# Performance work log

Hardware: AMD Instinct MI355X
Metric: run time of the kernel (lower is better)

Reference implementation:

```python
import jax, jax.numpy as jnp
import numpy as np

N, E = 100000, 1600000
IN, HID, NCLS = 128, 128, 64


def setup_inputs() -> dict:
    key = jax.random.key(0)
    ks = jax.random.split(key, 8)
    x = jax.random.normal(ks[0], (N, IN), jnp.float32)
    edge_index = jax.random.randint(ks[1], (2, E), 0, N, dtype=jnp.int32)
    s1 = 1.0 / np.sqrt(IN)
    s2 = 1.0 / np.sqrt(HID)
    return {
        "x": x,
        "edge_index": edge_index,
        "Wl1": jax.random.uniform(ks[2], (IN, HID), jnp.float32, -s1, s1),
        "Wr1": jax.random.uniform(ks[3], (IN, HID), jnp.float32, -s1, s1),
        "b1": jnp.zeros((HID,), jnp.float32),
        "Wl2": jax.random.uniform(ks[4], (HID, NCLS), jnp.float32, -s2, s2),
        "Wr2": jax.random.uniform(ks[5], (HID, NCLS), jnp.float32, -s2, s2),
        "b2": jnp.zeros((NCLS,), jnp.float32),
    }


def _sage_conv(x, src, dst, inv_deg, Wl, Wr, b):
    # mean-aggregate neighbor features at each destination node (PyG SAGEConv)
    agg = jax.ops.segment_sum(x[src], dst, num_segments=N)  # [N, d]
    agg = agg * inv_deg[:, None]
    # out = lin_l(mean_j x_j) + lin_r(x_i); bias lives in lin_l
    return agg @ Wl + x @ Wr + b


def reference(x, edge_index, Wl1, Wr1, b1, Wl2, Wr2, b2):
    src, dst = edge_index[0], edge_index[1]
    deg = jax.ops.segment_sum(jnp.ones((E,), jnp.float32), dst, num_segments=N)
    inv_deg = 1.0 / jnp.maximum(deg, 1.0)
    h = _sage_conv(x, src, dst, inv_deg, Wl1, Wr1, b1)
    h = jax.nn.relu(h)
    # dropout is identity at inference (training=False)
    h = _sage_conv(h, src, dst, inv_deg, Wl2, Wr2, b2)
    return jax.nn.log_softmax(h, axis=1)
```

## Files before the change

### kernel.cpp

```cpp
#include <hip/hip_runtime.h>
#include <hip/hip_bf16.h>


typedef __attribute__((ext_vector_type(8))) short short8;
typedef __attribute__((ext_vector_type(4))) float f32x4;
typedef __attribute__((ext_vector_type(2))) float f32x2;

#define NPB 512
#define BCAP 16384
#define CHUNK 8192

__device__ __forceinline__ ushort f2bf(float f) {
    unsigned u = __float_as_uint(f);
    return (ushort)((u + 0x7fff + ((u >> 16) & 1)) >> 16);
}
__device__ __forceinline__ float bflo(unsigned v) { return __uint_as_float(v << 16); }
__device__ __forceinline__ float bfhi(unsigned v) { return __uint_as_float(v & 0xffff0000u); }
__device__ __forceinline__ unsigned pk4bf(float a, float b) {
    return (unsigned)f2bf(a) | ((unsigned)f2bf(b) << 16);
}

__global__ void bucket_scatter(const int* __restrict__ src, const int* __restrict__ dst,
                               int* __restrict__ bcount, unsigned* __restrict__ bbuf,
                               int E, int NB) {
    __shared__ unsigned entry[CHUNK];
    __shared__ unsigned char ebkt[CHUNK];
    __shared__ int lhist[256], lbase[256], lcur[256];
    int tid = threadIdx.x;
    lhist[tid] = 0;
    __syncthreads();
    int e0 = blockIdx.x * CHUNK;
    int cnt = min(CHUNK, E - e0);
    int nv = cnt >> 2;
    for (int t = tid; t < nv; t += 256) {
        int4 d4 = ((const int4*)(dst + e0))[t];
        int4 s4 = ((const int4*)(src + e0))[t];
        int i = t * 4;
        int b0 = d4.x >> 9, b1 = d4.y >> 9, b2 = d4.z >> 9, b3 = d4.w >> 9;
        entry[i + 0] = ((unsigned)s4.x << 9) | (unsigned)(d4.x & 511);
        entry[i + 1] = ((unsigned)s4.y << 9) | (unsigned)(d4.y & 511);
        entry[i + 2] = ((unsigned)s4.z << 9) | (unsigned)(d4.z & 511);
        entry[i + 3] = ((unsigned)s4.w << 9) | (unsigned)(d4.w & 511);
        ebkt[i + 0] = (unsigned char)b0; ebkt[i + 1] = (unsigned char)b1;
        ebkt[i + 2] = (unsigned char)b2; ebkt[i + 3] = (unsigned char)b3;
        atomicAdd(&lhist[b0], 1); atomicAdd(&lhist[b1], 1);
        atomicAdd(&lhist[b2], 1); atomicAdd(&lhist[b3], 1);
    }
    for (int i = (nv << 2) + tid; i < cnt; i += 256) {
        int d = dst[e0 + i], s = src[e0 + i];
        int b = d >> 9;
        entry[i] = ((unsigned)s << 9) | (unsigned)(d & 511);
        ebkt[i] = (unsigned char)b;
        atomicAdd(&lhist[b], 1);
    }
    __syncthreads();
    int h = lhist[tid];
    lbase[tid] = (h > 0) ? atomicAdd(&bcount[tid], h) : 0;
    lcur[tid] = 0;
    __syncthreads();
    for (int i = tid; i < cnt; i += 256) {
        int b = ebkt[i];
        int o = atomicAdd(&lcur[b], 1);
        bbuf[(long)b * BCAP + lbase[b] + o] = entry[i];
    }
}

__global__ void scan_buckets(const int* __restrict__ bcount, int* __restrict__ bbase, int NB) {
    __shared__ int s[256];
    int tid = threadIdx.x;
    int v = (tid < NB) ? bcount[tid] : 0;
    s[tid] = v;
    __syncthreads();
    for (int off = 1; off < 256; off <<= 1) {
        int a = (tid >= off) ? s[tid - off] : 0;
        __syncthreads();
        s[tid] += a;
        __syncthreads();
    }
    if (tid < NB) bbase[tid] = s[tid] - v;
}

__global__ void build_csr(const unsigned* __restrict__ bbuf, const int* __restrict__ bcount,
                          const int* __restrict__ bbase, int* __restrict__ row_start,
                          int* __restrict__ degw, float* __restrict__ inv_deg,
                          int* __restrict__ ssrc, int N) {
    __shared__ int sdeg[NPB], lcur[NPB];
    int b = blockIdx.x, tid = threadIdx.x;
    int node0 = b * NPB;
    sdeg[tid] = 0; sdeg[tid + 256] = 0;
    __syncthreads();
    int cnt = bcount[b];
    long base = (long)b * BCAP;
    for (int i = tid; i < cnt; i += 256)
        atomicAdd(&sdeg[bbuf[base + i] & 511], 1);
    __syncthreads();
    int c0 = sdeg[tid], c1 = sdeg[tid + 256];
    for (int off = 1; off < NPB; off <<= 1) {
        int a0 = (tid >= off) ? sdeg[tid - off] : 0;
        int a1 = (tid + 256 >= off) ? sdeg[tid + 256 - off] : 0;
        __syncthreads();
        sdeg[tid] += a0; sdeg[tid + 256] += a1;
        __syncthreads();
    }
    int bb = bbase[b];
    int rs0 = bb + sdeg[tid] - c0;
    int rs1 = bb + sdeg[tid + 256] - c1;
    lcur[tid] = rs0; lcur[tid + 256] = rs1;
    if (node0 + tid < N) {
        row_start[node0 + tid] = rs0;
        degw[node0 + tid] = c0;
        inv_deg[node0 + tid] = 1.0f / (float)(c0 > 1 ? c0 : 1);
    }
    if (node0 + tid + 256 < N) {
        row_start[node0 + tid + 256] = rs1;
        degw[node0 + tid + 256] = c1;
        inv_deg[node0 + tid + 256] = 1.0f / (float)(c1 > 1 ? c1 : 1);
    }
    __syncthreads();
    for (int i = tid; i < cnt; i += 256) {
        unsigned w = bbuf[base + i];
        int pos = atomicAdd(&lcur[w & 511], 1);
        ssrc[pos] = (int)(w >> 9);
    }
}

__device__ __forceinline__ void wfrag_one(const float* W, ushort* Wf, int i, int COLS) {
    int j = i & 7, m = (i >> 3) & 15, kc = (i >> 7) & 15, ct = i >> 11;
    Wf[i] = f2bf(W[(kc * 8 + j) * COLS + ct * 16 + m]);
}
__global__ void cvt_w_kernel(const float* __restrict__ Wl1, const float* __restrict__ Wr1,
                             const float* __restrict__ Wl2, const float* __restrict__ Wr2,
                             ushort* __restrict__ Wf_l1, ushort* __restrict__ Wf_r1,
                             ushort* __restrict__ Wf_l2, ushort* __restrict__ Wf_r2) {
    int i = blockIdx.x * blockDim.x + threadIdx.x;
    if (i < 16384)       wfrag_one(Wl1, Wf_l1, i, 128);
    else if (i < 32768)  wfrag_one(Wr1, Wf_r1, i - 16384, 128);
    else if (i < 40960)  wfrag_one(Wl2, Wf_l2, i - 32768, 64);
    else if (i < 49152)  wfrag_one(Wr2, Wf_r2, i - 40960, 64);
}

template <int COLS, bool F32IN>
__global__ void proj_kernel(const void* __restrict__ xin,
                            const ushort* __restrict__ Wfl, const ushort* __restrict__ Wfr,
                            const float* __restrict__ bias,
                            unsigned char* __restrict__ p8,
                            ushort* __restrict__ q,
                            int N) {
    constexpr int CT = COLS / 16;
    int wave = threadIdx.x >> 6, lane = threadIdx.x & 63;
    int quad = lane >> 4, m = lane & 15;
    long row0 = (long)blockIdx.x * 64 + wave * 16;
    long node = row0 + m;
    long arow = (node < N) ? node : (N - 1);

    f32x4 accp[CT], accq[CT];
#pragma unroll
    for (int ct = 0; ct < CT; ++ct) { accp[ct] = (f32x4)0.0f; accq[ct] = (f32x4)0.0f; }

#pragma unroll
    for (int kk = 0; kk < 128; kk += 32) {
        short8 b;
        if (F32IN) {
            const float* xf = (const float*)xin + arow * 128 + kk + quad * 8;
            float4 f0 = *(const float4*)xf;
            float4 f1 = *(const float4*)(xf + 4);
            b[0] = (short)f2bf(f0.x); b[1] = (short)f2bf(f0.y);
            b[2] = (short)f2bf(f0.z); b[3] = (short)f2bf(f0.w);
            b[4] = (short)f2bf(f1.x); b[5] = (short)f2bf(f1.y);
            b[6] = (short)f2bf(f1.z); b[7] = (short)f2bf(f1.w);
        } else {
            b = *(const short8*)((const ushort*)xin + arow * 128 + kk + quad * 8);
        }
        int kc = (kk >> 3) + quad;
#pragma unroll
        for (int ct = 0; ct < CT; ++ct) {
            long boff = (((long)(ct * 16 + kc) * 16) + m) * 8;
            short8 al = *(const short8*)(Wfl + boff);
            short8 ar = *(const short8*)(Wfr + boff);
            accp[ct] = __builtin_amdgcn_mfma_f32_16x16x32_bf16(al, b, accp[ct], 0, 0, 0);
            accq[ct] = __builtin_amdgcn_mfma_f32_16x16x32_bf16(ar, b, accq[ct], 0, 0, 0);
        }
    }

    if (node < N) {
#pragma unroll
        for (int ct = 0; ct < CT; ++ct) {
            int c0 = ct * 16 + quad * 4;
            float4 bv = *(const float4*)(bias + c0);
            float q0 = accq[ct][0] + bv.x, q1 = accq[ct][1] + bv.y;
            float q2 = accq[ct][2] + bv.z, q3 = accq[ct][3] + bv.w;
            unsigned w = (unsigned)__builtin_amdgcn_cvt_pk_fp8_f32(accp[ct][0], accp[ct][1], 0, false);
            w = (unsigned)__builtin_amdgcn_cvt_pk_fp8_f32(accp[ct][2], accp[ct][3], (int)w, true);
            *(unsigned*)(p8 + node * COLS + c0) = w;
            uint2 qw; qw.x = pk4bf(q0, q1); qw.y = pk4bf(q2, q3);
            *(uint2*)(q + node * COLS + c0) = qw;
        }
    }
}

__global__ void agg_relu_kernel(const unsigned char* __restrict__ p8,
                                const ushort* __restrict__ q,
                                const int* __restrict__ ssrc,
                                const int* __restrict__ row_start,
                                const int* __restrict__ deg,
                                const float* __restrict__ inv_deg,
                                ushort* __restrict__ hb, int N) {
    int wave = threadIdx.x >> 6, lane = threadIdx.x & 63;
    int n = blockIdx.x * 4 + wave;
    if (n >= N) return;
    int g = lane >> 4, lm = lane & 15;
    int start = row_start[n], d = deg[n];
    const int* sp = ssrc + start;
    const unsigned char* pb = p8 + lm * 8;
    float a[8] = {};
    int j = 0;
    for (; j + 16 <= d; j += 16) {
        int s0 = sp[j + g], s1 = sp[j + 4 + g], s2 = sp[j + 8 + g], s3 = sp[j + 12 + g];
        uint2 v0 = *(const uint2*)(pb + (long)s0 * 128);
        uint2 v1 = *(const uint2*)(pb + (long)s1 * 128);
        uint2 v2 = *(const uint2*)(pb + (long)s2 * 128);
        uint2 v3 = *(const uint2*)(pb + (long)s3 * 128);
#pragma unroll
        for (int t = 0; t < 4; ++t) {
            uint2 vv = (t == 0) ? v0 : (t == 1) ? v1 : (t == 2) ? v2 : v3;
            f32x2 c0 = __builtin_amdgcn_cvt_pk_f32_fp8((int)vv.x, false);
            f32x2 c1 = __builtin_amdgcn_cvt_pk_f32_fp8((int)vv.x, true);
            f32x2 c2 = __builtin_amdgcn_cvt_pk_f32_fp8((int)vv.y, false);
            f32x2 c3 = __builtin_amdgcn_cvt_pk_f32_fp8((int)vv.y, true);
            a[0] += c0[0]; a[1] += c0[1]; a[2] += c1[0]; a[3] += c1[1];
            a[4] += c2[0]; a[5] += c2[1]; a[6] += c3[0]; a[7] += c3[1];
        }
    }
    for (; j < d; j += 4) {
        int idx = j + g;
        int s = sp[idx < d ? idx : j];
        uint2 vv = *(const uint2*)(pb + (long)s * 128);
        if (idx < d) {
            f32x2 c0 = __builtin_amdgcn_cvt_pk_f32_fp8((int)vv.x, false);
            f32x2 c1 = __builtin_amdgcn_cvt_pk_f32_fp8((int)vv.x, true);
            f32x2 c2 = __builtin_amdgcn_cvt_pk_f32_fp8((int)vv.y, false);
            f32x2 c3 = __builtin_amdgcn_cvt_pk_f32_fp8((int)vv.y, true);
            a[0] += c0[0]; a[1] += c0[1]; a[2] += c1[0]; a[3] += c1[1];
            a[4] += c2[0]; a[5] += c2[1]; a[6] += c3[0]; a[7] += c3[1];
        }
    }
#pragma unroll
    for (int t = 0; t < 8; ++t) {
        a[t] += __shfl_xor(a[t], 16);
        a[t] += __shfl_xor(a[t], 32);
    }
    if (g == 0) {
        float iv = inv_deg[n];
        uint4 qv = *(const uint4*)(q + (long)n * 128 + lm * 8);
        float h0 = fmaxf(a[0] * iv + bflo(qv.x), 0.f);
        float h1 = fmaxf(a[1] * iv + bfhi(qv.x), 0.f);
        float h2 = fmaxf(a[2] * iv + bflo(qv.y), 0.f);
        float h3 = fmaxf(a[3] * iv + bfhi(qv.y), 0.f);
        float h4 = fmaxf(a[4] * iv + bflo(qv.z), 0.f);
        float h5 = fmaxf(a[5] * iv + bfhi(qv.z), 0.f);
        float h6 = fmaxf(a[6] * iv + bflo(qv.w), 0.f);
        float h7 = fmaxf(a[7] * iv + bfhi(qv.w), 0.f);
        uint4 hw;
        hw.x = pk4bf(h0, h1); hw.y = pk4bf(h2, h3);
        hw.z = pk4bf(h4, h5); hw.w = pk4bf(h6, h7);
        *(uint4*)(hb + (long)n * 128 + lm * 8) = hw;
    }
}

__global__ void agg_lsm_kernel(const unsigned char* __restrict__ u8,
                               const ushort* __restrict__ v,
                               const int* __restrict__ ssrc,
                               const int* __restrict__ row_start,
                               const int* __restrict__ deg,
                               const float* __restrict__ inv_deg,
                               float* __restrict__ out, int N) {
    int wave = threadIdx.x >> 6, lane = threadIdx.x & 63;
    int n = blockIdx.x * 4 + wave;
    if (n >= N) return;
    int g = lane >> 3, lm = lane & 7;
    int start = row_start[n], d = deg[n];
    const int* sp = ssrc + start;
    const unsigned char* ub = u8 + lm * 8;
    float a[8] = {};
    int j = 0;
    for (; j + 16 <= d; j += 16) {
        int s0 = sp[j + g], s1 = sp[j + 8 + g];
        uint2 v0 = *(const uint2*)(ub + (long)s0 * 64);
        uint2 v1 = *(const uint2*)(ub + (long)s1 * 64);
#pragma unroll
        for (int t = 0; t < 2; ++t) {
            uint2 vv = (t == 0) ? v0 : v1;
            f32x2 c0 = __builtin_amdgcn_cvt_pk_f32_fp8((int)vv.x, false);
            f32x2 c1 = __builtin_amdgcn_cvt_pk_f32_fp8((int)vv.x, true);
            f32x2 c2 = __builtin_amdgcn_cvt_pk_f32_fp8((int)vv.y, false);
            f32x2 c3 = __builtin_amdgcn_cvt_pk_f32_fp8((int)vv.y, true);
            a[0] += c0[0]; a[1] += c0[1]; a[2] += c1[0]; a[3] += c1[1];
            a[4] += c2[0]; a[5] += c2[1]; a[6] += c3[0]; a[7] += c3[1];
        }
    }
    for (; j < d; j += 8) {
        int idx = j + g;
        int s = sp[idx < d ? idx : j];
        uint2 vv = *(const uint2*)(ub + (long)s * 64);
        if (idx < d) {
            f32x2 c0 = __builtin_amdgcn_cvt_pk_f32_fp8((int)vv.x, false);
            f32x2 c1 = __builtin_amdgcn_cvt_pk_f32_fp8((int)vv.x, true);
            f32x2 c2 = __builtin_amdgcn_cvt_pk_f32_fp8((int)vv.y, false);
            f32x2 c3 = __builtin_amdgcn_cvt_pk_f32_fp8((int)vv.y, true);
            a[0] += c0[0]; a[1] += c0[1]; a[2] += c1[0]; a[3] += c1[1];
            a[4] += c2[0]; a[5] += c2[1]; a[6] += c3[0]; a[7] += c3[1];
        }
    }
#pragma unroll
    for (int t = 0; t < 8; ++t) {
        a[t] += __shfl_xor(a[t], 8);
        a[t] += __shfl_xor(a[t], 16);
        a[t] += __shfl_xor(a[t], 32);
    }
    float iv = inv_deg[n];
    uint4 vv = *(const uint4*)(v + (long)n * 64 + lm * 8);
    float z0 = a[0] * iv + bflo(vv.x), z1 = a[1] * iv + bfhi(vv.x);
    float z2 = a[2] * iv + bflo(vv.y), z3 = a[3] * iv + bfhi(vv.y);
    float z4 = a[4] * iv + bflo(vv.z), z5 = a[5] * iv + bfhi(vv.z);
    float z6 = a[6] * iv + bflo(vv.w), z7 = a[7] * iv + bfhi(vv.w);
    float mx = fmaxf(fmaxf(fmaxf(z0, z1), fmaxf(z2, z3)),
                     fmaxf(fmaxf(z4, z5), fmaxf(z6, z7)));
#pragma unroll
    for (int o = 4; o > 0; o >>= 1) mx = fmaxf(mx, __shfl_xor(mx, o));
    float e = (__expf(z0 - mx) + __expf(z1 - mx)) + (__expf(z2 - mx) + __expf(z3 - mx)) +
              (__expf(z4 - mx) + __expf(z5 - mx)) + (__expf(z6 - mx) + __expf(z7 - mx));
#pragma unroll
    for (int o = 4; o > 0; o >>= 1) e += __shfl_xor(e, o);
    float ls = mx + __logf(e);
    if (g == 0) {
        float4 o0, o1;
        o0.x = z0 - ls; o0.y = z1 - ls; o0.z = z2 - ls; o0.w = z3 - ls;
        o1.x = z4 - ls; o1.y = z5 - ls; o1.z = z6 - ls; o1.w = z7 - ls;
        *(float4*)(out + (long)n * 64 + lm * 8) = o0;
        *(float4*)(out + (long)n * 64 + lm * 8 + 4) = o1;
    }
}

extern "C" void kernel_launch(void* const* d_in, const int* in_sizes, int n_in,
                              void* d_out, int out_size, void* d_ws, size_t ws_size,
                              hipStream_t stream) {
    const float* x   = (const float*)d_in[0];
    const int*   ei  = (const int*)d_in[1];
    const float* Wl1 = (const float*)d_in[2];
    const float* Wr1 = (const float*)d_in[3];
    const float* b1  = (const float*)d_in[4];
    const float* Wl2 = (const float*)d_in[5];
    const float* Wr2 = (const float*)d_in[6];
    const float* b2  = (const float*)d_in[7];

    const int N = in_sizes[0] / 128;
    const int E = in_sizes[1] / 2;
    const int* src = ei;
    const int* dst = ei + E;
    const int NB = (N + NPB - 1) / NPB;

    size_t off = 0;
    auto take = [&](size_t nbytes) -> void* {
        void* ptr = (void*)((char*)d_ws + off);
        off += (nbytes + 255) & ~(size_t)255;
        return ptr;
    };
    int*      bcount    = (int*)take((size_t)NB * 4);
    int*      bbase     = (int*)take((size_t)NB * 4);
    unsigned* bbuf      = (unsigned*)take((size_t)NB * BCAP * 4);
    int*      row_start = (int*)take((size_t)N * 4);
    int*      degw      = (int*)take((size_t)N * 4);
    float*    inv_deg   = (float*)take((size_t)N * 4);
    int*      ssrc      = (int*)take((size_t)E * 4);
    unsigned char* p8   = (unsigned char*)take((size_t)N * 128);
    ushort*   q         = (ushort*)take((size_t)N * 128 * 2);
    ushort*   hb        = (ushort*)take((size_t)N * 128 * 2);
    ushort*   Wf_l1     = (ushort*)take(128 * 128 * 2);
    ushort*   Wf_r1     = (ushort*)take(128 * 128 * 2);
    ushort*   Wf_l2     = (ushort*)take(64 * 128 * 2);
    ushort*   Wf_r2     = (ushort*)take(64 * 128 * 2);
    unsigned char* u8 = p8;
    ushort*        v  = q;
    (void)ws_size; (void)n_in; (void)out_size;

    hipMemsetAsync(bcount, 0, (size_t)NB * 4, stream);

    bucket_scatter<<<(E + CHUNK - 1) / CHUNK, 256, 0, stream>>>(src, dst, bcount, bbuf, E, NB);
    scan_buckets  <<<1, 256, 0, stream>>>(bcount, bbase, NB);
    build_csr     <<<NB, 256, 0, stream>>>(bbuf, bcount, bbase, row_start, degw, inv_deg, ssrc, N);
    cvt_w_kernel  <<<192, 256, 0, stream>>>(Wl1, Wr1, Wl2, Wr2, Wf_l1, Wf_r1, Wf_l2, Wf_r2);

    proj_kernel<128, true><<<(N + 63) / 64, 256, 0, stream>>>(x, Wf_l1, Wf_r1, b1, p8, q, N);
    agg_relu_kernel<<<(N + 3) / 4, 256, 0, stream>>>(p8, q, ssrc, row_start, degw, inv_deg, hb, N);

    proj_kernel<64, false><<<(N + 63) / 64, 256, 0, stream>>>(hb, Wf_l2, Wf_r2, b2, u8, v, N);
    agg_lsm_kernel<<<(N + 3) / 4, 256, 0, stream>>>(u8, v, ssrc, row_start, degw, inv_deg,
                                                    (float*)d_out, N);
}
```

Baseline: 297.5 us.

## Widen gather loads to 16 bytes, shuffle-broadcast edge indices, merge scan with weight conversion

Both aggregation kernels now give each lane 16 fp8 features per 16-byte load, so fewer lanes cover a row and more edges are gathered per wave step. Each wave loads up to 64 neighbor indices in one coalesced read and hands them out with __shfl, replacing repeated scalar index loads. Accumulators become packed float2, and the bucket scan and weight-fragment conversion share one launch. The cost is more lanes idle on the masked tail for low-degree nodes, more shuffle reduction steps, and heavier per-lane epilogues.

```diff
diff --git a/kernel.cpp b/kernel.cpp
--- a/kernel.cpp
+++ b/kernel.cpp
@@ -18,6 +18,19 @@
 __device__ __forceinline__ float bfhi(unsigned v) { return __uint_as_float(v & 0xffff0000u); }
 __device__ __forceinline__ unsigned pk4bf(float a, float b) {
     return (unsigned)f2bf(a) | ((unsigned)f2bf(b) << 16);
+}
+__device__ __forceinline__ f32x2 shflx2(f32x2 v, int m) {
+    f32x2 r; r[0] = __shfl_xor(v[0], m); r[1] = __shfl_xor(v[1], m); return r;
+}
+__device__ __forceinline__ void acc16(uint4 v, f32x2* a) {
+    a[0] += __builtin_amdgcn_cvt_pk_f32_fp8((int)v.x, false);
+    a[1] += __builtin_amdgcn_cvt_pk_f32_fp8((int)v.x, true);
+    a[2] += __builtin_amdgcn_cvt_pk_f32_fp8((int)v.y, false);
+    a[3] += __builtin_amdgcn_cvt_pk_f32_fp8((int)v.y, true);
+    a[4] += __builtin_amdgcn_cvt_pk_f32_fp8((int)v.z, false);
+    a[5] += __builtin_amdgcn_cvt_pk_f32_fp8((int)v.z, true);
+    a[6] += __builtin_amdgcn_cvt_pk_f32_fp8((int)v.w, false);
+    a[7] += __builtin_amdgcn_cvt_pk_f32_fp8((int)v.w, true);
 }
 
 __global__ void bucket_scatter(const int* __restrict__ src, const int* __restrict__ dst,
@@ -65,19 +78,36 @@
     }
 }
 
-__global__ void scan_buckets(const int* __restrict__ bcount, int* __restrict__ bbase, int NB) {
-    __shared__ int s[256];
+__device__ __forceinline__ void wfrag_one(const float* W, ushort* Wf, int i, int COLS) {
+    int j = i & 7, m = (i >> 3) & 15, kc = (i >> 7) & 15, ct = i >> 11;
+    Wf[i] = f2bf(W[(kc * 8 + j) * COLS + ct * 16 + m]);
+}
+__global__ void scan_cvtw_kernel(const int* __restrict__ bcount, int* __restrict__ bbase,
+                                 int NB,
+                                 const float* __restrict__ Wl1, const float* __restrict__ Wr1,
+                                 const float* __restrict__ Wl2, const float* __restrict__ Wr2,
+                                 ushort* __restrict__ Wf_l1, ushort* __restrict__ Wf_r1,
+                                 ushort* __restrict__ Wf_l2, ushort* __restrict__ Wf_r2) {
     int tid = threadIdx.x;
-    int v = (tid < NB) ? bcount[tid] : 0;
-    s[tid] = v;
-    __syncthreads();
-    for (int off = 1; off < 256; off <<= 1) {
-        int a = (tid >= off) ? s[tid - off] : 0;
+    if (blockIdx.x == 0) {
+        __shared__ int s[256];
+        int v = (tid < NB) ? bcount[tid] : 0;
+        s[tid] = v;
         __syncthreads();
-        s[tid] += a;
-        __syncthreads();
-    }
-    if (tid < NB) bbase[tid] = s[tid] - v;
+        for (int off = 1; off < 256; off <<= 1) {
+            int a = (tid >= off) ? s[tid - off] : 0;
+            __syncthreads();
+            s[tid] += a;
+            __syncthreads();
+        }
+        if (tid < NB) bbase[tid] = s[tid] - v;
+        return;
+    }
+    int i = (int)(blockIdx.x - 1) * 256 + tid;
+    if (i < 16384)       wfrag_one(Wl1, Wf_l1, i, 128);
+    else if (i < 32768)  wfrag_one(Wr1, Wf_r1, i - 16384, 128);
+    else if (i < 40960)  wfrag_one(Wl2, Wf_l2, i - 32768, 64);
+    else if (i < 49152)  wfrag_one(Wr2, Wf_r2, i - 40960, 64);
 }
 
 __global__ void build_csr(const unsigned* __restrict__ bbuf, const int* __restrict__ bcount,
@@ -124,32 +154,16 @@
     }
 }
 
-__device__ __forceinline__ void wfrag_one(const float* W, ushort* Wf, int i, int COLS) {
-    int j = i & 7, m = (i >> 3) & 15, kc = (i >> 7) & 15, ct = i >> 11;
-    Wf[i] = f2bf(W[(kc * 8 + j) * COLS + ct * 16 + m]);
-}
-__global__ void cvt_w_kernel(const float* __restrict__ Wl1, const float* __restrict__ Wr1,
-                             const float* __restrict__ Wl2, const float* __restrict__ Wr2,
-                             ushort* __restrict__ Wf_l1, ushort* __restrict__ Wf_r1,
-                             ushort* __restrict__ Wf_l2, ushort* __restrict__ Wf_r2) {
-    int i = blockIdx.x * blockDim.x + threadIdx.x;
-    if (i < 16384)       wfrag_one(Wl1, Wf_l1, i, 128);
-    else if (i < 32768)  wfrag_one(Wr1, Wf_r1, i - 16384, 128);
-    else if (i < 40960)  wfrag_one(Wl2, Wf_l2, i - 32768, 64);
-    else if (i < 49152)  wfrag_one(Wr2, Wf_r2, i - 40960, 64);
-}
-
 template <int COLS, bool F32IN>
-__global__ void proj_kernel(const void* __restrict__ xin,
+__device__ __forceinline__ void proj_body(int bid, int tid,
+                            const void* __restrict__ xin,
                             const ushort* __restrict__ Wfl, const ushort* __restrict__ Wfr,
                             const float* __restrict__ bias,
-                            unsigned char* __restrict__ p8,
-                            ushort* __restrict__ q,
-                            int N) {
+                            unsigned char* __restrict__ p8, ushort* __restrict__ q, int N) {
     constexpr int CT = COLS / 16;
-    int wave = threadIdx.x >> 6, lane = threadIdx.x & 63;
+    int wave = tid >> 6, lane = tid & 63;
     int quad = lane >> 4, m = lane & 15;
-    long row0 = (long)blockIdx.x * 64 + wave * 16;
+    long row0 = (long)bid * 64 + wave * 16;
     long node = row0 + m;
     long arow = (node < N) ? node : (N - 1);
 
@@ -198,146 +212,153 @@
     }
 }
 
-__global__ void agg_relu_kernel(const unsigned char* __restrict__ p8,
-                                const ushort* __restrict__ q,
-                                const int* __restrict__ ssrc,
-                                const int* __restrict__ row_start,
-                                const int* __restrict__ deg,
-                                const float* __restrict__ inv_deg,
-                                ushort* __restrict__ hb, int N) {
-    int wave = threadIdx.x >> 6, lane = threadIdx.x & 63;
-    int n = blockIdx.x * 4 + wave;
-    if (n >= N) return;
-    int g = lane >> 4, lm = lane & 15;
-    int start = row_start[n], d = deg[n];
-    const int* sp = ssrc + start;
-    const unsigned char* pb = p8 + lm * 8;
-    float a[8] = {};
-    int j = 0;
-    for (; j + 16 <= d; j += 16) {
-        int s0 = sp[j + g], s1 = sp[j + 4 + g], s2 = sp[j + 8 + g], s3 = sp[j + 12 + g];
-        uint2 v0 = *(const uint2*)(pb + (long)s0 * 128);
-        uint2 v1 = *(const uint2*)(pb + (long)s1 * 128);
-        uint2 v2 = *(const uint2*)(pb + (long)s2 * 128);
-        uint2 v3 = *(const uint2*)(pb + (long)s3 * 128);
-#pragma unroll
-        for (int t = 0; t < 4; ++t) {
-            uint2 vv = (t == 0) ? v0 : (t == 1) ? v1 : (t == 2) ? v2 : v3;
-            f32x2 c0 = __builtin_amdgcn_cvt_pk_f32_fp8((int)vv.x, false);
-            f32x2 c1 = __builtin_amdgcn_cvt_pk_f32_fp8((int)vv.x, true);
-            f32x2 c2 = __builtin_amdgcn_cvt_pk_f32_fp8((int)vv.y, false);
-            f32x2 c3 = __builtin_amdgcn_cvt_pk_f32_fp8((int)vv.y, true);
-            a[0] += c0[0]; a[1] += c0[1]; a[2] += c1[0]; a[3] += c1[1];
-            a[4] += c2[0]; a[5] += c2[1]; a[6] += c3[0]; a[7] += c3[1];
-        }
-    }
-    for (; j < d; j += 4) {
-        int idx = j + g;
-        int s = sp[idx < d ? idx : j];
-        uint2 vv = *(const uint2*)(pb + (long)s * 128);
-        if (idx < d) {
-            f32x2 c0 = __builtin_amdgcn_cvt_pk_f32_fp8((int)vv.x, false);
-            f32x2 c1 = __builtin_amdgcn_cvt_pk_f32_fp8((int)vv.x, true);
-            f32x2 c2 = __builtin_amdgcn_cvt_pk_f32_fp8((int)vv.y, false);
-            f32x2 c3 = __builtin_amdgcn_cvt_pk_f32_fp8((int)vv.y, true);
-            a[0] += c0[0]; a[1] += c0[1]; a[2] += c1[0]; a[3] += c1[1];
-            a[4] += c2[0]; a[5] += c2[1]; a[6] += c3[0]; a[7] += c3[1];
-        }
-    }
-#pragma unroll
-    for (int t = 0; t < 8; ++t) {
-        a[t] += __shfl_xor(a[t], 16);
-        a[t] += __shfl_xor(a[t], 32);
-    }
-    if (g == 0) {
-        float iv = inv_deg[n];
-        uint4 qv = *(const uint4*)(q + (long)n * 128 + lm * 8);
-        float h0 = fmaxf(a[0] * iv + bflo(qv.x), 0.f);
-        float h1 = fmaxf(a[1] * iv + bfhi(qv.x), 0.f);
-        float h2 = fmaxf(a[2] * iv + bflo(qv.y), 0.f);
-        float h3 = fmaxf(a[3] * iv + bfhi(qv.y), 0.f);
-        float h4 = fmaxf(a[4] * iv + bflo(qv.z), 0.f);
-        float h5 = fmaxf(a[5] * iv + bfhi(qv.z), 0.f);
-        float h6 = fmaxf(a[6] * iv + bflo(qv.w), 0.f);
-        float h7 = fmaxf(a[7] * iv + bfhi(qv.w), 0.f);
-        uint4 hw;
-        hw.x = pk4bf(h0, h1); hw.y = pk4bf(h2, h3);
-        hw.z = pk4bf(h4, h5); hw.w = pk4bf(h6, h7);
-        *(uint4*)(hb + (long)n * 128 + lm * 8) = hw;
-    }
-}
-
-__global__ void agg_lsm_kernel(const unsigned char* __restrict__ u8,
-                               const ushort* __restrict__ v,
-                               const int* __restrict__ ssrc,
-                               const int* __restrict__ row_start,
-                               const int* __restrict__ deg,
-                               const float* __restrict__ inv_deg,
-                               float* __restrict__ out, int N) {
+__global__ void __launch_bounds__(256)
+proj1_kernel(const float* __restrict__ x,
+             const ushort* __restrict__ Wfl, const ushort* __restrict__ Wfr,
+             const float* __restrict__ bias,
+             unsigned char* __restrict__ p8, ushort* __restrict__ q, int N) {
+    proj_body<128, true>((int)blockIdx.x, (int)threadIdx.x, x, Wfl, Wfr, bias, p8, q, N);
+}
+__global__ void __launch_bounds__(256)
+proj2_kernel(const ushort* __restrict__ hb,
+             const ushort* __restrict__ Wfl, const ushort* __restrict__ Wfr,
+             const float* __restrict__ bias,
+             unsigned char* __restrict__ u8, ushort* __restrict__ v, int N) {
+    proj_body<64, false>((int)blockIdx.x, (int)threadIdx.x, hb, Wfl, Wfr, bias, u8, v, N);
+}
+
+__global__ void __launch_bounds__(256)
+agg_relu_kernel(const unsigned char* __restrict__ p8,
+                const ushort* __restrict__ q,
+                const int* __restrict__ ssrc,
+                const int* __restrict__ row_start,
+                const int* __restrict__ deg,
+                const float* __restrict__ inv_deg,
+                ushort* __restrict__ hb, int N) {
     int wave = threadIdx.x >> 6, lane = threadIdx.x & 63;
     int n = blockIdx.x * 4 + wave;
     if (n >= N) return;
     int g = lane >> 3, lm = lane & 7;
     int start = row_start[n], d = deg[n];
     const int* sp = ssrc + start;
-    const unsigned char* ub = u8 + lm * 8;
-    float a[8] = {};
-    int j = 0;
-    for (; j + 16 <= d; j += 16) {
-        int s0 = sp[j + g], s1 = sp[j + 8 + g];
-        uint2 v0 = *(const uint2*)(ub + (long)s0 * 64);
-        uint2 v1 = *(const uint2*)(ub + (long)s1 * 64);
-#pragma unroll
-        for (int t = 0; t < 2; ++t) {
-            uint2 vv = (t == 0) ? v0 : v1;
-            f32x2 c0 = __builtin_amdgcn_cvt_pk_f32_fp8((int)vv.x, false);
-            f32x2 c1 = __builtin_amdgcn_cvt_pk_f32_fp8((int)vv.x, true);
-            f32x2 c2 = __builtin_amdgcn_cvt_pk_f32_fp8((int)vv.y, false);
-            f32x2 c3 = __builtin_amdgcn_cvt_pk_f32_fp8((int)vv.y, true);
-            a[0] += c0[0]; a[1] += c0[1]; a[2] += c1[0]; a[3] += c1[1];
-            a[4] += c2[0]; a[5] += c2[1]; a[6] += c3[0]; a[7] += c3[1];
-        }
-    }
-    for (; j < d; j += 8) {
-        int idx = j + g;
-        int s = sp[idx < d ? idx : j];
-        uint2 vv = *(const uint2*)(ub + (long)s * 64);
-        if (idx < d) {
-            f32x2 c0 = __builtin_amdgcn_cvt_pk_f32_fp8((int)vv.x, false);
-            f32x2 c1 = __builtin_amdgcn_cvt_pk_f32_fp8((int)vv.x, true);
-            f32x2 c2 = __builtin_amdgcn_cvt_pk_f32_fp8((int)vv.y, false);
-            f32x2 c3 = __builtin_amdgcn_cvt_pk_f32_fp8((int)vv.y, true);
-            a[0] += c0[0]; a[1] += c0[1]; a[2] += c1[0]; a[3] += c1[1];
-            a[4] += c2[0]; a[5] += c2[1]; a[6] += c3[0]; a[7] += c3[1];
+    const unsigned char* pb = p8 + lm * 16;
+    f32x2 a[8] = {};
+    for (int w = 0; w < d; w += 64) {
+        int rem = d - w;
+        int li = lane < rem ? lane : rem - 1;
+        int idxv = sp[w + li];
+        int iters = rem < 64 ? rem : 64;
+        for (int e0 = 0; e0 < iters; e0 += 16) {
+            int eA = e0 + g, eB = e0 + 8 + g;
+            int sA = __shfl(idxv, eA < iters ? eA : 0);
+            int sB = __shfl(idxv, eB < iters ? eB : 0);
+            uint4 vA = *(const uint4*)(pb + (long)sA * 128);
+            uint4 vB = *(const uint4*)(pb + (long)sB * 128);
+            if (eA >= iters) vA = make_uint4(0, 0, 0, 0);
+            if (eB >= iters) vB = make_uint4(0, 0, 0, 0);
+            acc16(vA, a);
+            acc16(vB, a);
         }
     }
 #pragma unroll
     for (int t = 0; t < 8; ++t) {
-        a[t] += __shfl_xor(a[t], 8);
-        a[t] += __shfl_xor(a[t], 16);
-        a[t] += __shfl_xor(a[t], 32);
+        a[t] += shflx2(a[t], 8);
+        a[t] += shflx2(a[t], 16);
+        a[t] += shflx2(a[t], 32);
+    }
+    if (g == 0) {
+        float iv = inv_deg[n];
+        const uint4* qp = (const uint4*)(q + (long)n * 128 + lm * 16);
+        uint4 qa = qp[0], qb = qp[1];
+        unsigned qd[8] = {qa.x, qa.y, qa.z, qa.w, qb.x, qb.y, qb.z, qb.w};
+        float hv[16];
+#pragma unroll
+        for (int j = 0; j < 16; ++j) hv[j] = a[j >> 1][j & 1] * iv;
+#pragma unroll
+        for (int j = 0; j < 8; ++j) {
+            hv[2 * j]     = fmaxf(hv[2 * j] + bflo(qd[j]), 0.f);
+            hv[2 * j + 1] = fmaxf(hv[2 * j + 1] + bfhi(qd[j]), 0.f);
+        }
+        uint4 ha, hbv;
+        ha.x = pk4bf(hv[0], hv[1]);   ha.y = pk4bf(hv[2], hv[3]);
+        ha.z = pk4bf(hv[4], hv[5]);   ha.w = pk4bf(hv[6], hv[7]);
+        hbv.x = pk4bf(hv[8], hv[9]);  hbv.y = pk4bf(hv[10], hv[11]);
+        hbv.z = pk4bf(hv[12], hv[13]); hbv.w = pk4bf(hv[14], hv[15]);
+        uint4* hp = (uint4*)(hb + (long)n * 128 + lm * 16);
+        hp[0] = ha; hp[1] = hbv;
+    }
+}
+
+__global__ void __launch_bounds__(256)
+agg_lsm_kernel(const unsigned char* __restrict__ u8,
+               const ushort* __restrict__ vt,
+               const int* __restrict__ ssrc,
+               const int* __restrict__ row_start,
+               const int* __restrict__ deg,
+               const float* __restrict__ inv_deg,
+               float* __restrict__ out, int N) {
+    int wave = threadIdx.x >> 6, lane = threadIdx.x & 63;
+    int n = blockIdx.x * 4 + wave;
+    if (n >= N) return;
+    int g = lane >> 2, lm = lane & 3;
+    int start = row_start[n], d = deg[n];
+    const int* sp = ssrc + start;
+    const unsigned char* ub = u8 + lm * 16;
+    f32x2 a[8] = {};
+    for (int w = 0; w < d; w += 64) {
+        int rem = d - w;
+        int li = lane < rem ? lane : rem - 1;
+        int idxv = sp[w + li];
+        int iters = rem < 64 ? rem : 64;
+        for (int e0 = 0; e0 < iters; e0 += 32) {
+            int eA = e0 + g, eB = e0 + 16 + g;
+            int sA = __shfl(idxv, eA < iters ? eA : 0);
+            int sB = __shfl(idxv, eB < iters ? eB : 0);
+            uint4 vA = *(const uint4*)(ub + (long)sA * 64);
+            uint4 vB = *(const uint4*)(ub + (long)sB * 64);
+            if (eA >= iters) vA = make_uint4(0, 0, 0, 0);
+            if (eB >= iters) vB = make_uint4(0, 0, 0, 0);
+            acc16(vA, a);
+            acc16(vB, a);
+        }
+    }
+#pragma unroll
+    for (int t = 0; t < 8; ++t) {
+        a[t] += shflx2(a[t], 4);
+        a[t] += shflx2(a[t], 8);
+        a[t] += shflx2(a[t], 16);
+        a[t] += shflx2(a[t], 32);
     }
     float iv = inv_deg[n];
-    uint4 vv = *(const uint4*)(v + (long)n * 64 + lm * 8);
-    float z0 = a[0] * iv + bflo(vv.x), z1 = a[1] * iv + bfhi(vv.x);
-    float z2 = a[2] * iv + bflo(vv.y), z3 = a[3] * iv + bfhi(vv.y);
-    float z4 = a[4] * iv + bflo(vv.z), z5 = a[5] * iv + bfhi(vv.z);
-    float z6 = a[6] * iv + bflo(vv.w), z7 = a[7] * iv + bfhi(vv.w);
-    float mx = fmaxf(fmaxf(fmaxf(z0, z1), fmaxf(z2, z3)),
-                     fmaxf(fmaxf(z4, z5), fmaxf(z6, z7)));
-#pragma unroll
-    for (int o = 4; o > 0; o >>= 1) mx = fmaxf(mx, __shfl_xor(mx, o));
-    float e = (__expf(z0 - mx) + __expf(z1 - mx)) + (__expf(z2 - mx) + __expf(z3 - mx)) +
-              (__expf(z4 - mx) + __expf(z5 - mx)) + (__expf(z6 - mx) + __expf(z7 - mx));
-#pragma unroll
-    for (int o = 4; o > 0; o >>= 1) e += __shfl_xor(e, o);
-    float ls = mx + __logf(e);
+    const uint4* vp = (const uint4*)(vt + (long)n * 64 + lm * 16);
+    uint4 va = vp[0], vb = vp[1];
+    unsigned vd[8] = {va.x, va.y, va.z, va.w, vb.x, vb.y, vb.z, vb.w};
+    float z[16];
+#pragma unroll
+    for (int j = 0; j < 8; ++j) {
+        z[2 * j]     = a[j][0] * iv + bflo(vd[j]);
+        z[2 * j + 1] = a[j][1] * iv + bfhi(vd[j]);
+    }
+    float mx = z[0];
+#pragma unroll
+    for (int j = 1; j < 16; ++j) mx = fmaxf(mx, z[j]);
+    mx = fmaxf(mx, __shfl_xor(mx, 1));
+    mx = fmaxf(mx, __shfl_xor(mx, 2));
+    float es = 0.f;
+#pragma unroll
+    for (int j = 0; j < 16; ++j) es += __expf(z[j] - mx);
+    es += __shfl_xor(es, 1);
+    es += __shfl_xor(es, 2);
+    float ls = mx + __logf(es);
     if (g == 0) {
-        float4 o0, o1;
-        o0.x = z0 - ls; o0.y = z1 - ls; o0.z = z2 - ls; o0.w = z3 - ls;
-        o1.x = z4 - ls; o1.y = z5 - ls; o1.z = z6 - ls; o1.w = z7 - ls;
-        *(float4*)(out + (long)n * 64 + lm * 8) = o0;
-        *(float4*)(out + (long)n * 64 + lm * 8 + 4) = o1;
+        float* op = out + (long)n * 64 + lm * 16;
+#pragma unroll
+        for (int j4 = 0; j4 < 4; ++j4) {
+            float4 o4;
+            o4.x = z[j4 * 4 + 0] - ls; o4.y = z[j4 * 4 + 1] - ls;
+            o4.z = z[j4 * 4 + 2] - ls; o4.w = z[j4 * 4 + 3] - ls;
+            *(float4*)(op + j4 * 4) = o4;
+        }
     }
 }
 
@@ -386,14 +407,15 @@
     hipMemsetAsync(bcount, 0, (size_t)NB * 4, stream);
 
     bucket_scatter<<<(E + CHUNK - 1) / CHUNK, 256, 0, stream>>>(src, dst, bcount, bbuf, E, NB);
-    scan_buckets  <<<1, 256, 0, stream>>>(bcount, bbase, NB);
-    build_csr     <<<NB, 256, 0, stream>>>(bbuf, bcount, bbase, row_start, degw, inv_deg, ssrc, N);
-    cvt_w_kernel  <<<192, 256, 0, stream>>>(Wl1, Wr1, Wl2, Wr2, Wf_l1, Wf_r1, Wf_l2, Wf_r2);
-
-    proj_kernel<128, true><<<(N + 63) / 64, 256, 0, stream>>>(x, Wf_l1, Wf_r1, b1, p8, q, N);
+    scan_cvtw_kernel<<<1 + 192, 256, 0, stream>>>(bcount, bbase, NB,
+                                                  Wl1, Wr1, Wl2, Wr2,
+                                                  Wf_l1, Wf_r1, Wf_l2, Wf_r2);
+    build_csr<<<NB, 256, 0, stream>>>(bbuf, bcount, bbase, row_start, degw, inv_deg, ssrc, N);
+
+    proj1_kernel<<<(N + 63) / 64, 256, 0, stream>>>(x, Wf_l1, Wf_r1, b1, p8, q, N);
     agg_relu_kernel<<<(N + 3) / 4, 256, 0, stream>>>(p8, q, ssrc, row_start, degw, inv_deg, hb, N);
 
-    proj_kernel<64, false><<<(N + 63) / 64, 256, 0, stream>>>(hb, Wf_l2, Wf_r2, b2, u8, v, N);
+    proj2_kernel<<<(N + 63) / 64, 256, 0, stream>>>(hb, Wf_l2, Wf_r2, b2, u8, v, N);
     agg_lsm_kernel<<<(N + 3) / 4, 256, 0, stream>>>(u8, v, ssrc, row_start, degw, inv_deg,
                                                     (float*)d_out, N);
 }
```

Result: slower. 339.1 us (+14.0%).

## Merge preprocessing kernels and drop bucket scan via padded CSR layout

Applied to the files above, without the earlier changes.

Folds the weight conversion into the bucket scatter launch and the layer-1 projection into the CSR build launch, using block-index ranges so the independent work runs side by side. The global bucket scan kernel is removed by giving each bucket a fixed BCAP-sized region in ssrc, so row_start points into that padded array. Aggregation accumulators switch to packed float2 vectors so the adds and shuffles can use packed ops. This cuts two launches and a serial step, at the cost of a larger ssrc buffer and a hard per-bucket capacity limit.

```diff
diff --git a/kernel.cpp b/kernel.cpp
--- a/kernel.cpp
+++ b/kernel.cpp
@@ -19,14 +19,34 @@
 __device__ __forceinline__ unsigned pk4bf(float a, float b) {
     return (unsigned)f2bf(a) | ((unsigned)f2bf(b) << 16);
 }
-
-__global__ void bucket_scatter(const int* __restrict__ src, const int* __restrict__ dst,
-                               int* __restrict__ bcount, unsigned* __restrict__ bbuf,
-                               int E, int NB) {
+__device__ __forceinline__ f32x2 shflx2(f32x2 v, int m) {
+    f32x2 r; r[0] = __shfl_xor(v[0], m); r[1] = __shfl_xor(v[1], m); return r;
+}
+
+__device__ __forceinline__ void wfrag_one(const float* W, ushort* Wf, int i, int COLS) {
+    int j = i & 7, m = (i >> 3) & 15, kc = (i >> 7) & 15, ct = i >> 11;
+    Wf[i] = f2bf(W[(kc * 8 + j) * COLS + ct * 16 + m]);
+}
+
+__global__ void __launch_bounds__(256)
+k1_scatter_cvtw(const int* __restrict__ src, const int* __restrict__ dst,
+                int* __restrict__ bcount, unsigned* __restrict__ bbuf, int E, int NSC,
+                const float* __restrict__ Wl1, const float* __restrict__ Wr1,
+                const float* __restrict__ Wl2, const float* __restrict__ Wr2,
+                ushort* __restrict__ Wf_l1, ushort* __restrict__ Wf_r1,
+                ushort* __restrict__ Wf_l2, ushort* __restrict__ Wf_r2) {
+    int tid = threadIdx.x;
+    if ((int)blockIdx.x >= NSC) {
+        int i = ((int)blockIdx.x - NSC) * 256 + tid;
+        if (i < 16384)       wfrag_one(Wl1, Wf_l1, i, 128);
+        else if (i < 32768)  wfrag_one(Wr1, Wf_r1, i - 16384, 128);
+        else if (i < 40960)  wfrag_one(Wl2, Wf_l2, i - 32768, 64);
+        else if (i < 49152)  wfrag_one(Wr2, Wf_r2, i - 40960, 64);
+        return;
+    }
     __shared__ unsigned entry[CHUNK];
     __shared__ unsigned char ebkt[CHUNK];
     __shared__ int lhist[256], lbase[256], lcur[256];
-    int tid = threadIdx.x;
     lhist[tid] = 0;
     __syncthreads();
     int e0 = blockIdx.x * CHUNK;
@@ -65,91 +85,16 @@
     }
 }
 
-__global__ void scan_buckets(const int* __restrict__ bcount, int* __restrict__ bbase, int NB) {
-    __shared__ int s[256];
-    int tid = threadIdx.x;
-    int v = (tid < NB) ? bcount[tid] : 0;
-    s[tid] = v;
-    __syncthreads();
-    for (int off = 1; off < 256; off <<= 1) {
-        int a = (tid >= off) ? s[tid - off] : 0;
-        __syncthreads();
-        s[tid] += a;
-        __syncthreads();
-    }
-    if (tid < NB) bbase[tid] = s[tid] - v;
-}
-
-__global__ void build_csr(const unsigned* __restrict__ bbuf, const int* __restrict__ bcount,
-                          const int* __restrict__ bbase, int* __restrict__ row_start,
-                          int* __restrict__ degw, float* __restrict__ inv_deg,
-                          int* __restrict__ ssrc, int N) {
-    __shared__ int sdeg[NPB], lcur[NPB];
-    int b = blockIdx.x, tid = threadIdx.x;
-    int node0 = b * NPB;
-    sdeg[tid] = 0; sdeg[tid + 256] = 0;
-    __syncthreads();
-    int cnt = bcount[b];
-    long base = (long)b * BCAP;
-    for (int i = tid; i < cnt; i += 256)
-        atomicAdd(&sdeg[bbuf[base + i] & 511], 1);
-    __syncthreads();
-    int c0 = sdeg[tid], c1 = sdeg[tid + 256];
-    for (int off = 1; off < NPB; off <<= 1) {
-        int a0 = (tid >= off) ? sdeg[tid - off] : 0;
-        int a1 = (tid + 256 >= off) ? sdeg[tid + 256 - off] : 0;
-        __syncthreads();
-        sdeg[tid] += a0; sdeg[tid + 256] += a1;
-        __syncthreads();
-    }
-    int bb = bbase[b];
-    int rs0 = bb + sdeg[tid] - c0;
-    int rs1 = bb + sdeg[tid + 256] - c1;
-    lcur[tid] = rs0; lcur[tid + 256] = rs1;
-    if (node0 + tid < N) {
-        row_start[node0 + tid] = rs0;
-        degw[node0 + tid] = c0;
-        inv_deg[node0 + tid] = 1.0f / (float)(c0 > 1 ? c0 : 1);
-    }
-    if (node0 + tid + 256 < N) {
-        row_start[node0 + tid + 256] = rs1;
-        degw[node0 + tid + 256] = c1;
-        inv_deg[node0 + tid + 256] = 1.0f / (float)(c1 > 1 ? c1 : 1);
-    }
-    __syncthreads();
-    for (int i = tid; i < cnt; i += 256) {
-        unsigned w = bbuf[base + i];
-        int pos = atomicAdd(&lcur[w & 511], 1);
-        ssrc[pos] = (int)(w >> 9);
-    }
-}
-
-__device__ __forceinline__ void wfrag_one(const float* W, ushort* Wf, int i, int COLS) {
-    int j = i & 7, m = (i >> 3) & 15, kc = (i >> 7) & 15, ct = i >> 11;
-    Wf[i] = f2bf(W[(kc * 8 + j) * COLS + ct * 16 + m]);
-}
-__global__ void cvt_w_kernel(const float* __restrict__ Wl1, const float* __restrict__ Wr1,
-                             const float* __restrict__ Wl2, const float* __restrict__ Wr2,
-                             ushort* __restrict__ Wf_l1, ushort* __restrict__ Wf_r1,
-                             ushort* __restrict__ Wf_l2, ushort* __restrict__ Wf_r2) {
-    int i = blockIdx.x * blockDim.x + threadIdx.x;
-    if (i < 16384)       wfrag_one(Wl1, Wf_l1, i, 128);
-    else if (i < 32768)  wfrag_one(Wr1, Wf_r1, i - 16384, 128);
-    else if (i < 40960)  wfrag_one(Wl2, Wf_l2, i - 32768, 64);
-    else if (i < 49152)  wfrag_one(Wr2, Wf_r2, i - 40960, 64);
-}
-
 template <int COLS, bool F32IN>
-__global__ void proj_kernel(const void* __restrict__ xin,
+__device__ __forceinline__ void proj_body(int bid, int tid,
+                            const void* __restrict__ xin,
                             const ushort* __restrict__ Wfl, const ushort* __restrict__ Wfr,
                             const float* __restrict__ bias,
-                            unsigned char* __restrict__ p8,
-                            ushort* __restrict__ q,
-                            int N) {
+                            unsigned char* __restrict__ p8, ushort* __restrict__ q, int N) {
     constexpr int CT = COLS / 16;
-    int wave = threadIdx.x >> 6, lane = threadIdx.x & 63;
+    int wave = tid >> 6, lane = tid & 63;
     int quad = lane >> 4, m = lane & 15;
-    long row0 = (long)blockIdx.x * 64 + wave * 16;
+    long row0 = (long)bid * 64 + wave * 16;
     long node = row0 + m;
     long arow = (node < N) ? node : (N - 1);
 
@@ -198,13 +143,66 @@
     }
 }
 
-__global__ void agg_relu_kernel(const unsigned char* __restrict__ p8,
-                                const ushort* __restrict__ q,
-                                const int* __restrict__ ssrc,
-                                const int* __restrict__ row_start,
-                                const int* __restrict__ deg,
-                                const float* __restrict__ inv_deg,
-                                ushort* __restrict__ hb, int N) {
+__global__ void __launch_bounds__(256)
+k2_csr_proj1(const unsigned* __restrict__ bbuf, const int* __restrict__ bcount,
+             int* __restrict__ row_start, int* __restrict__ degw,
+             float* __restrict__ inv_deg, int* __restrict__ ssrc, int NBcsr, int N,
+             const float* __restrict__ x,
+             const ushort* __restrict__ Wfl, const ushort* __restrict__ Wfr,
+             const float* __restrict__ bias,
+             unsigned char* __restrict__ p8, ushort* __restrict__ q) {
+    int tid = threadIdx.x;
+    if ((int)blockIdx.x >= NBcsr) {
+        proj_body<128, true>((int)blockIdx.x - NBcsr, tid, x, Wfl, Wfr, bias, p8, q, N);
+        return;
+    }
+    __shared__ int sdeg[NPB], lcur[NPB];
+    int b = blockIdx.x;
+    int node0 = b * NPB;
+    sdeg[tid] = 0; sdeg[tid + 256] = 0;
+    __syncthreads();
+    int cnt = bcount[b];
+    long base = (long)b * BCAP;
+    for (int i = tid; i < cnt; i += 256)
+        atomicAdd(&sdeg[bbuf[base + i] & 511], 1);
+    __syncthreads();
+    int c0 = sdeg[tid], c1 = sdeg[tid + 256];
+    for (int off = 1; off < NPB; off <<= 1) {
+        int a0 = (tid >= off) ? sdeg[tid - off] : 0;
+        int a1 = (tid + 256 >= off) ? sdeg[tid + 256 - off] : 0;
+        __syncthreads();
+        sdeg[tid] += a0; sdeg[tid + 256] += a1;
+        __syncthreads();
+    }
+    int rs0 = sdeg[tid] - c0;
+    int rs1 = sdeg[tid + 256] - c1;
+    lcur[tid] = rs0; lcur[tid + 256] = rs1;
+    if (node0 + tid < N) {
+        row_start[node0 + tid] = (int)(base + rs0);
+        degw[node0 + tid] = c0;
+        inv_deg[node0 + tid] = 1.0f / (float)(c0 > 1 ? c0 : 1);
+    }
+    if (node0 + tid + 256 < N) {
+        row_start[node0 + tid + 256] = (int)(base + rs1);
+        degw[node0 + tid + 256] = c1;
+        inv_deg[node0 + tid + 256] = 1.0f / (float)(c1 > 1 ? c1 : 1);
+    }
+    __syncthreads();
+    for (int i = tid; i < cnt; i += 256) {
+        unsigned w = bbuf[base + i];
+        int pos = atomicAdd(&lcur[w & 511], 1);
+        ssrc[base + pos] = (int)(w >> 9);
+    }
+}
+
+__global__ void __launch_bounds__(256)
+agg_relu_kernel(const unsigned char* __restrict__ p8,
+                const ushort* __restrict__ q,
+                const int* __restrict__ ssrc,
+                const int* __restrict__ row_start,
+                const int* __restrict__ deg,
+                const float* __restrict__ inv_deg,
+                ushort* __restrict__ hb, int N) {
     int wave = threadIdx.x >> 6, lane = threadIdx.x & 63;
     int n = blockIdx.x * 4 + wave;
     if (n >= N) return;
@@ -212,7 +210,7 @@
     int start = row_start[n], d = deg[n];
     const int* sp = ssrc + start;
     const unsigned char* pb = p8 + lm * 8;
-    float a[8] = {};
+    f32x2 a0 = (f32x2)0.f, a1 = (f32x2)0.f, a2 = (f32x2)0.f, a3 = (f32x2)0.f;
     int j = 0;
     for (; j + 16 <= d; j += 16) {
         int s0 = sp[j + g], s1 = sp[j + 4 + g], s2 = sp[j + 8 + g], s3 = sp[j + 12 + g];
@@ -223,12 +221,10 @@
 #pragma unroll
         for (int t = 0; t < 4; ++t) {
             uint2 vv = (t == 0) ? v0 : (t == 1) ? v1 : (t == 2) ? v2 : v3;
-            f32x2 c0 = __builtin_amdgcn_cvt_pk_f32_fp8((int)vv.x, false);
-            f32x2 c1 = __builtin_amdgcn_cvt_pk_f32_fp8((int)vv.x, true);
-            f32x2 c2 = __builtin_amdgcn_cvt_pk_f32_fp8((int)vv.y, false);
-            f32x2 c3 = __builtin_amdgcn_cvt_pk_f32_fp8((int)vv.y, true);
-            a[0] += c0[0]; a[1] += c0[1]; a[2] += c1[0]; a[3] += c1[1];
-            a[4] += c2[0]; a[5] += c2[1]; a[6] += c3[0]; a[7] += c3[1];
+            a0 += __builtin_amdgcn_cvt_pk_f32_fp8((int)vv.x, false);
+            a1 += __builtin_amdgcn_cvt_pk_f32_fp8((int)vv.x, true);
+            a2 += __builtin_amdgcn_cvt_pk_f32_fp8((int)vv.y, false);
+            a3 += __builtin_amdgcn_cvt_pk_f32_fp8((int)vv.y, true);
         }
     }
     for (; j < d; j += 4) {
@@ -236,30 +232,27 @@
         int s = sp[idx < d ? idx : j];
         uint2 vv = *(const uint2*)(pb + (long)s * 128);
         if (idx < d) {
-            f32x2 c0 = __builtin_amdgcn_cvt_pk_f32_fp8((int)vv.x, false);
-            f32x2 c1 = __builtin_amdgcn_cvt_pk_f32_fp8((int)vv.x, true);
-            f32x2 c2 = __builtin_amdgcn_cvt_pk_f32_fp8((int)vv.y, false);
-            f32x2 c3 = __builtin_amdgcn_cvt_pk_f32_fp8((int)vv.y, true);
-            a[0] += c0[0]; a[1] += c0[1]; a[2] += c1[0]; a[3] += c1[1];
-            a[4] += c2[0]; a[5] += c2[1]; a[6] += c3[0]; a[7] += c3[1];
-        }
-    }
-#pragma unroll
-    for (int t = 0; t < 8; ++t) {
-        a[t] += __shfl_xor(a[t], 16);
-        a[t] += __shfl_xor(a[t], 32);
-    }
+            a0 += __builtin_amdgcn_cvt_pk_f32_fp8((int)vv.x, false);
+            a1 += __builtin_amdgcn_cvt_pk_f32_fp8((int)vv.x, true);
+            a2 += __builtin_amdgcn_cvt_pk_f32_fp8((int)vv.y, false);
+            a3 += __builtin_amdgcn_cvt_pk_f32_fp8((int)vv.y, true);
+        }
+    }
+    a0 += shflx2(a0, 16); a1 += shflx2(a1, 16);
+    a2 += shflx2(a2, 16); a3 += shflx2(a3, 16);
+    a0 += shflx2(a0, 32); a1 += shflx2(a1, 32);
+    a2 += shflx2(a2, 32); a3 += shflx2(a3, 32);
     if (g == 0) {
         float iv = inv_deg[n];
         uint4 qv = *(const uint4*)(q + (long)n * 128 + lm * 8);
-        float h0 = fmaxf(a[0] * iv + bflo(qv.x), 0.f);
-        float h1 = fmaxf(a[1] * iv + bfhi(qv.x), 0.f);
-        float h2 = fmaxf(a[2] * iv + bflo(qv.y), 0.f);
-        float h3 = fmaxf(a[3] * iv + bfhi(qv.y), 0.f);
-        float h4 = fmaxf(a[4] * iv + bflo(qv.z), 0.f);
-        float h5 = fmaxf(a[5] * iv + bfhi(qv.z), 0.f);
-        float h6 = fmaxf(a[6] * iv + bflo(qv.w), 0.f);
-        float h7 = fmaxf(a[7] * iv + bfhi(qv.w), 0.f);
+        float h0 = fmaxf(a0[0] * iv + bflo(qv.x), 0.f);
+        float h1 = fmaxf(a0[1] * iv + bfhi(qv.x), 0.f);
+        float h2 = fmaxf(a1[0] * iv + bflo(qv.y), 0.f);
+        float h3 = fmaxf(a1[1] * iv + bfhi(qv.y), 0.f);
+        float h4 = fmaxf(a2[0] * iv + bflo(qv.z), 0.f);
+        float h5 = fmaxf(a2[1] * iv + bfhi(qv.z), 0.f);
+        float h6 = fmaxf(a3[0] * iv + bflo(qv.w), 0.f);
+        float h7 = fmaxf(a3[1] * iv + bfhi(qv.w), 0.f);
         uint4 hw;
         hw.x = pk4bf(h0, h1); hw.y = pk4bf(h2, h3);
         hw.z = pk4bf(h4, h5); hw.w = pk4bf(h6, h7);
@@ -267,13 +260,22 @@
     }
 }
 
-__global__ void agg_lsm_kernel(const unsigned char* __restrict__ u8,
-                               const ushort* __restrict__ v,
-                               const int* __restrict__ ssrc,
-                               const int* __restrict__ row_start,
-                               const int* __restrict__ deg,
-                               const float* __restrict__ inv_deg,
-                               float* __restrict__ out, int N) {
+__global__ void __launch_bounds__(256)
+proj2_kernel(const ushort* __restrict__ hb,
+             const ushort* __restrict__ Wfl, const ushort* __restrict__ Wfr,
+             const float* __restrict__ bias,
+             unsigned char* __restrict__ u8, ushort* __restrict__ v, int N) {
+    proj_body<64, false>((int)blockIdx.x, (int)threadIdx.x, hb, Wfl, Wfr, bias, u8, v, N);
+}
+
+__global__ void __launch_bounds__(256)
+agg_lsm_kernel(const unsigned char* __restrict__ u8,
+               const ushort* __restrict__ v,
+               const int* __restrict__ ssrc,
+               const int* __restrict__ row_start,
+               const int* __restrict__ deg,
+               const float* __restrict__ inv_deg,
+               float* __restrict__ out, int N) {
     int wave = threadIdx.x >> 6, lane = threadIdx.x & 63;
     int n = blockIdx.x * 4 + wave;
     if (n >= N) return;
@@ -281,7 +283,7 @@
     int start = row_start[n], d = deg[n];
     const int* sp = ssrc + start;
     const unsigned char* ub = u8 + lm * 8;
-    float a[8] = {};
+    f32x2 a0 = (f32x2)0.f, a1 = (f32x2)0.f, a2 = (f32x2)0.f, a3 = (f32x2)0.f;
     int j = 0;
     for (; j + 16 <= d; j += 16) {
         int s0 = sp[j + g], s1 = sp[j + 8 + g];
@@ -290,12 +292,10 @@
 #pragma unroll
         for (int t = 0; t < 2; ++t) {
             uint2 vv = (t == 0) ? v0 : v1;
-            f32x2 c0 = __builtin_amdgcn_cvt_pk_f32_fp8((int)vv.x, false);
-            f32x2 c1 = __builtin_amdgcn_cvt_pk_f32_fp8((int)vv.x, true);
-            f32x2 c2 = __builtin_amdgcn_cvt_pk_f32_fp8((int)vv.y, false);
-            f32x2 c3 = __builtin_amdgcn_cvt_pk_f32_fp8((int)vv.y, true);
-            a[0] += c0[0]; a[1] += c0[1]; a[2] += c1[0]; a[3] += c1[1];
-            a[4] += c2[0]; a[5] += c2[1]; a[6] += c3[0]; a[7] += c3[1];
+            a0 += __builtin_amdgcn_cvt_pk_f32_fp8((int)vv.x, false);
+            a1 += __builtin_amdgcn_cvt_pk_f32_fp8((int)vv.x, true);
+            a2 += __builtin_amdgcn_cvt_pk_f32_fp8((int)vv.y, false);
+            a3 += __builtin_amdgcn_cvt_pk_f32_fp8((int)vv.y, true);
         }
     }
     for (; j < d; j += 8) {
@@ -303,26 +303,22 @@
         int s = sp[idx < d ? idx : j];
         uint2 vv = *(const uint2*)(ub + (long)s * 64);
         if (idx < d) {
-            f32x2 c0 = __builtin_amdgcn_cvt_pk_f32_fp8((int)vv.x, false);
-            f32x2 c1 = __builtin_amdgcn_cvt_pk_f32_fp8((int)vv.x, true);
-            f32x2 c2 = __builtin_amdgcn_cvt_pk_f32_fp8((int)vv.y, false);
-            f32x2 c3 = __builtin_amdgcn_cvt_pk_f32_fp8((int)vv.y, true);
-            a[0] += c0[0]; a[1] += c0[1]; a[2] += c1[0]; a[3] += c1[1];
-            a[4] += c2[0]; a[5] += c2[1]; a[6] += c3[0]; a[7] += c3[1];
-        }
-    }
-#pragma unroll
-    for (int t = 0; t < 8; ++t) {
-        a[t] += __shfl_xor(a[t], 8);
-        a[t] += __shfl_xor(a[t], 16);
-        a[t] += __shfl_xor(a[t], 32);
-    }
+            a0 += __builtin_amdgcn_cvt_pk_f32_fp8((int)vv.x, false);
+            a1 += __builtin_amdgcn_cvt_pk_f32_fp8((int)vv.x, true);
+            a2 += __builtin_amdgcn_cvt_pk_f32_fp8((int)vv.y, false);
+            a3 += __builtin_amdgcn_cvt_pk_f32_fp8((int)vv.y, true);
+        }
+    }
+    a0 += shflx2(a0, 8);  a1 += shflx2(a1, 8);  a2 += shflx2(a2, 8);  a3 += shflx2(a3, 8);
+    a0 += shflx2(a0, 16); a1 += shflx2(a1, 16); a2 += shflx2(a2, 16); a3 += shflx2(a3, 16);
+    a0 += shflx2(a0, 32); a1 += shflx2(a1, 32); a2 += shflx2(a2, 32); a3 += shflx2(a3, 32);
+
     float iv = inv_deg[n];
     uint4 vv = *(const uint4*)(v + (long)n * 64 + lm * 8);
-    float z0 = a[0] * iv + bflo(vv.x), z1 = a[1] * iv + bfhi(vv.x);
-    float z2 = a[2] * iv + bflo(vv.y), z3 = a[3] * iv + bfhi(vv.y);
-    float z4 = a[4] * iv + bflo(vv.z), z5 = a[5] * iv + bfhi(vv.z);
-    float z6 = a[6] * iv + bflo(vv.w), z7 = a[7] * iv + bfhi(vv.w);
+    float z0 = a0[0] * iv + bflo(vv.x), z1 = a0[1] * iv + bfhi(vv.x);
+    float z2 = a1[0] * iv + bflo(vv.y), z3 = a1[1] * iv + bfhi(vv.y);
+    float z4 = a2[0] * iv + bflo(vv.z), z5 = a2[1] * iv + bfhi(vv.z);
+    float z6 = a3[0] * iv + bflo(vv.w), z7 = a3[1] * iv + bfhi(vv.w);
     float mx = fmaxf(fmaxf(fmaxf(z0, z1), fmaxf(z2, z3)),
                      fmaxf(fmaxf(z4, z5), fmaxf(z6, z7)));
 #pragma unroll
@@ -358,6 +354,7 @@
     const int* src = ei;
     const int* dst = ei + E;
     const int NB = (N + NPB - 1) / NPB;
+    const int NSC = (E + CHUNK - 1) / CHUNK;
 
     size_t off = 0;
     auto take = [&](size_t nbytes) -> void* {
@@ -366,12 +363,11 @@
         return ptr;
     };
     int*      bcount    = (int*)take((size_t)NB * 4);
-    int*      bbase     = (int*)take((size_t)NB * 4);
     unsigned* bbuf      = (unsigned*)take((size_t)NB * BCAP * 4);
     int*      row_start = (int*)take((size_t)N * 4);
     int*      degw      = (int*)take((size_t)N * 4);
     float*    inv_deg   = (float*)take((size_t)N * 4);
-    int*      ssrc      = (int*)take((size_t)E * 4);
+    int*      ssrc      = (int*)take((size_t)NB * BCAP * 4);
     unsigned char* p8   = (unsigned char*)take((size_t)N * 128);
     ushort*   q         = (ushort*)take((size_t)N * 128 * 2);
     ushort*   hb        = (ushort*)take((size_t)N * 128 * 2);
@@ -385,15 +381,17 @@
 
     hipMemsetAsync(bcount, 0, (size_t)NB * 4, stream);
 
-    bucket_scatter<<<(E + CHUNK - 1) / CHUNK, 256, 0, stream>>>(src, dst, bcount, bbuf, E, NB);
-    scan_buckets  <<<1, 256, 0, stream>>>(bcount, bbase, NB);
-    build_csr     <<<NB, 256, 0, stream>>>(bbuf, bcount, bbase, row_start, degw, inv_deg, ssrc, N);
-    cvt_w_kernel  <<<192, 256, 0, stream>>>(Wl1, Wr1, Wl2, Wr2, Wf_l1, Wf_r1, Wf_l2, Wf_r2);
-
-    proj_kernel<128, true><<<(N + 63) / 64, 256, 0, stream>>>(x, Wf_l1, Wf_r1, b1, p8, q, N);
+    k1_scatter_cvtw<<<NSC + 192, 256, 0, stream>>>(src, dst, bcount, bbuf, E, NSC,
+                                                   Wl1, Wr1, Wl2, Wr2,
+                                                   Wf_l1, Wf_r1, Wf_l2, Wf_r2);
+
+    int P1 = (N + 63) / 64;
+    k2_csr_proj1<<<NB + P1, 256, 0, stream>>>(bbuf, bcount, row_start, degw, inv_deg,
+                                              ssrc, NB, N, x, Wf_l1, Wf_r1, b1, p8, q);
+
     agg_relu_kernel<<<(N + 3) / 4, 256, 0, stream>>>(p8, q, ssrc, row_start, degw, inv_deg, hb, N);
 
-    proj_kernel<64, false><<<(N + 63) / 64, 256, 0, stream>>>(hb, Wf_l2, Wf_r2, b2, u8, v, N);
+    proj2_kernel<<<(N + 63) / 64, 256, 0, stream>>>(hb, Wf_l2, Wf_r2, b2, u8, v, N);
     agg_lsm_kernel<<<(N + 3) / 4, 256, 0, stream>>>(u8, v, ssrc, row_start, degw, inv_deg,
                                                     (float*)d_out, N);
 }
```

New measurement: 285.7 us. 4.0% less time.
